# Kernel tuning notes

Hardware: AMD Instinct MI355X
Metric: run time of the kernel (lower is better)

Reference implementation:

```python
import jax, jax.numpy as jnp
import numpy as np


def setup_inputs() -> dict:
    key = jax.random.key(0)
    inputs = jax.random.normal(key, (4, 1024, 64), dtype=jnp.float32)
    return {"inputs": inputs}


def reference(inputs):
    # inputs: (B, N, D)
    # scores[b,i,j] = sum_d tanh(x[b,i,d] + x[b,j,d])
    addition = inputs[:, :, None, :] + inputs[:, None, :, :]  # (B, N, N, D)
    e_values = jnp.tanh(addition).sum(axis=-1)                # (B, N, N)
    weights = jax.nn.softmax(e_values, axis=-1)               # (B, N, N)
    out = jnp.einsum("bij,bjd->bid", weights, inputs)         # (B, N, D)
    return out
```

## Files before the change

### kernel.cpp

```cpp
#include <hip/hip_runtime.h>


#define NB 4
#define NN 1024
#define ND 64
#define TJ 64
#define TI 4
#define NTILES (NN / TJ)

#if __has_builtin(__builtin_amdgcn_exp2f)
#define EXP2F(x) __builtin_amdgcn_exp2f(x)
#else
#define EXP2F(x) exp2f(x)
#endif
#if __has_builtin(__builtin_amdgcn_rcpf)
#define RCPF(x) __builtin_amdgcn_rcpf(x)
#else
#define RCPF(x) (1.0f / (x))
#endif

static constexpr float C_SCALE = 2.8853900817779268f;
static constexpr float K_SHIFT = 46.166241308446828f;

typedef float v2f __attribute__((ext_vector_type(2)));

#define PKFMA(a, b, c) __builtin_elementwise_fma((a), (b), (c))

__device__ __forceinline__ v2f vlo(float4 v) { v2f r; r.x = v.x; r.y = v.y; return r; }
__device__ __forceinline__ v2f vhi(float4 v) { v2f r; r.x = v.z; r.y = v.w; return r; }

__global__ __launch_bounds__(256) void prep_kernel(const float* __restrict__ x,
                                                   float* __restrict__ E) {
    int idx = blockIdx.x * 256 + threadIdx.x;
    float4 v = ((const float4*)x)[idx];
    float4 e;
    e.x = EXP2F(C_SCALE * v.x);
    e.y = EXP2F(C_SCALE * v.y);
    e.z = EXP2F(C_SCALE * v.z);
    e.w = EXP2F(C_SCALE * v.w);
    ((float4*)E)[idx] = e;
}

template <bool HAS_E>
__global__ __launch_bounds__(256, 4) void addattn_kernel(const float* __restrict__ x,
                                                         const float* __restrict__ E,
                                                         float* __restrict__ out) {
    __shared__ float E_lds[TJ * ND];
    __shared__ float x_lds[TJ * ND];

    const int tid   = threadIdx.x;
    const int lane  = tid & 63;
    const int wave  = tid >> 6;
    const int wg    = blockIdx.x;
    const int b     = wg >> 8;
    const int ibase = (wg & 255) * TI;
    const int i0    = __builtin_amdgcn_readfirstlane(ibase + wave);

    const float* xb  = x + (size_t)b * NN * ND;
    const float* Eip = E + (size_t)b * NN * ND + (size_t)i0 * ND;

    float4 px[4];
    {
        const float4* srcx = (const float4*)xb;
        #pragma unroll
        for (int it = 0; it < 4; ++it) px[it] = srcx[it * 256 + tid];
    }

    v2f ei2[32];
    if (!HAS_E) {
        #pragma unroll
        for (int c = 0; c < 16; ++c) {
            float4 xiq = *(const float4*)&xb[(size_t)i0 * ND + c * 4];
            v2f lo, hi;
            lo.x = EXP2F(C_SCALE * xiq.x);
            lo.y = EXP2F(C_SCALE * xiq.y);
            hi.x = EXP2F(C_SCALE * xiq.z);
            hi.y = EXP2F(C_SCALE * xiq.w);
            ei2[2 * c] = lo;
            ei2[2 * c + 1] = hi;
        }
    }

    #pragma unroll
    for (int it = 0; it < 4; ++it) {
        int idx = it * 256 + tid;
        int j   = idx >> 4;
        int c   = idx & 15;
        int wof = j * ND + ((c ^ (j & 15)) << 2);
        *(float4*)&x_lds[wof] = px[it];
        float4 ev;
        ev.x = EXP2F(C_SCALE * px[it].x);
        ev.y = EXP2F(C_SCALE * px[it].y);
        ev.z = EXP2F(C_SCALE * px[it].z);
        ev.w = EXP2F(C_SCALE * px[it].w);
        *(float4*)&E_lds[wof] = ev;
    }
    __syncthreads();

    v2f acc2[32];
    #pragma unroll
    for (int k = 0; k < 32; ++k) acc2[k] = (v2f){0.f, 0.f};
    float dn = 0.f;

    for (int t = 0; t < NTILES; ++t) {
        if (t + 1 < NTILES) {
            const float4* srcx = (const float4*)(xb + (size_t)(t + 1) * TJ * ND);
            #pragma unroll
            for (int it = 0; it < 4; ++it) px[it] = srcx[it * 256 + tid];
        }

        const int key = lane & 15;
        v2f rse = {0.f, 0.f}, rso = {0.f, 0.f};
        #pragma unroll
        for (int c = 0; c < 16; ++c) {
            float4 ejq = *(const float4*)&E_lds[lane * ND + ((c ^ key) << 2)];
            v2f eil, eih;
            if (HAS_E) {
                float4 eiq = *(const float4*)&Eip[c * 4];
                eil = vlo(eiq); eih = vhi(eiq);
            } else {
                eil = ei2[2 * c]; eih = ei2[2 * c + 1];
            }
            v2f a = eil * vlo(ejq);
            v2f q = eih * vhi(ejq);
            v2f p = a + q;
            v2f r = PKFMA(a, q, p + 1.0f);
            v2f tt; tt.x = RCPF(r.x); tt.y = RCPF(r.y);
            if (c & 1) rso = PKFMA(p + 2.0f, tt, rso);
            else       rse = PKFMA(p + 2.0f, tt, rse);
        }
        v2f rs = rse + rso;
        float w = EXP2F(fmaf(-C_SCALE, rs.x + rs.y, K_SHIFT));
        dn += w;
        v2f w2; w2.x = w; w2.y = w;

        #pragma unroll
        for (int c = 0; c < 16; ++c) {
            float4 xq = *(const float4*)&x_lds[lane * ND + ((c ^ key) << 2)];
            acc2[2 * c]     = PKFMA(w2, vlo(xq), acc2[2 * c]);
            acc2[2 * c + 1] = PKFMA(w2, vhi(xq), acc2[2 * c + 1]);
        }

        if (t + 1 < NTILES) {
            __syncthreads();
            #pragma unroll
            for (int it = 0; it < 4; ++it) {
                int idx = it * 256 + tid;
                int j   = idx >> 4;
                int c   = idx & 15;
                int wof = j * ND + ((c ^ (j & 15)) << 2);
                *(float4*)&x_lds[wof] = px[it];
                float4 ev;
                ev.x = EXP2F(C_SCALE * px[it].x);
                ev.y = EXP2F(C_SCALE * px[it].y);
                ev.z = EXP2F(C_SCALE * px[it].z);
                ev.w = EXP2F(C_SCALE * px[it].w);
                *(float4*)&E_lds[wof] = ev;
            }
            __syncthreads();
        }
    }

    float* accf = (float*)acc2;
    #pragma unroll
    for (int s = 0; s < 6; ++s) {
        const int half = 32 >> s;
        const int sel  = (lane >> (5 - s)) & 1;
        #pragma unroll
        for (int k = 0; k < half; ++k) {
            float keep = sel ? accf[k + half] : accf[k];
            float send = sel ? accf[k] : accf[k + half];
            float recv = __shfl_xor(send, half, 64);
            accf[k] = keep + recv;
        }
    }
    #pragma unroll
    for (int s = 0; s < 6; ++s) dn += __shfl_xor(dn, 1 << s, 64);

    out[((size_t)b * NN + i0) * ND + lane] = accf[0] * RCPF(dn);
}

extern "C" void kernel_launch(void* const* d_in, const int* in_sizes, int n_in,
                              void* d_out, int out_size, void* d_ws, size_t ws_size,
                              hipStream_t stream) {
    const float* x = (const float*)d_in[0];
    float* out = (float*)d_out;
    const size_t e_bytes = (size_t)NB * NN * ND * sizeof(float);

    dim3 grid(NB * (NN / TI));
    dim3 block(256);

    if (ws_size >= e_bytes) {
        float* E = (float*)d_ws;
        prep_kernel<<<dim3(NB * NN * ND / 4 / 256), dim3(256), 0, stream>>>(x, E);
        addattn_kernel<true><<<grid, block, 0, stream>>>(x, E, out);
    } else {
        addattn_kernel<false><<<grid, block, 0, stream>>>(x, (const float*)nullptr, out);
    }
}
```

Baseline: 67.98 us.

## Compute exp of sum directly per pair, drop E precompute and LDS tile

```diff
diff --git a/kernel.cpp b/kernel.cpp
--- a/kernel.cpp
+++ b/kernel.cpp
@@ -29,23 +29,8 @@
 __device__ __forceinline__ v2f vlo(float4 v) { v2f r; r.x = v.x; r.y = v.y; return r; }
 __device__ __forceinline__ v2f vhi(float4 v) { v2f r; r.x = v.z; r.y = v.w; return r; }
 
-__global__ __launch_bounds__(256) void prep_kernel(const float* __restrict__ x,
-                                                   float* __restrict__ E) {
-    int idx = blockIdx.x * 256 + threadIdx.x;
-    float4 v = ((const float4*)x)[idx];
-    float4 e;
-    e.x = EXP2F(C_SCALE * v.x);
-    e.y = EXP2F(C_SCALE * v.y);
-    e.z = EXP2F(C_SCALE * v.z);
-    e.w = EXP2F(C_SCALE * v.w);
-    ((float4*)E)[idx] = e;
-}
-
-template <bool HAS_E>
-__global__ __launch_bounds__(256, 4) void addattn_kernel(const float* __restrict__ x,
-                                                         const float* __restrict__ E,
+__global__ __launch_bounds__(256, 2) void addattn_kernel(const float* __restrict__ x,
                                                          float* __restrict__ out) {
-    __shared__ float E_lds[TJ * ND];
     __shared__ float x_lds[TJ * ND];
 
     const int tid   = threadIdx.x;
@@ -57,7 +42,7 @@
     const int i0    = __builtin_amdgcn_readfirstlane(ibase + wave);
 
     const float* xb  = x + (size_t)b * NN * ND;
-    const float* Eip = E + (size_t)b * NN * ND + (size_t)i0 * ND;
+    const float* xip = xb + (size_t)i0 * ND;
 
     float4 px[4];
     {
@@ -65,35 +50,12 @@
         #pragma unroll
         for (int it = 0; it < 4; ++it) px[it] = srcx[it * 256 + tid];
     }
-
-    v2f ei2[32];
-    if (!HAS_E) {
-        #pragma unroll
-        for (int c = 0; c < 16; ++c) {
-            float4 xiq = *(const float4*)&xb[(size_t)i0 * ND + c * 4];
-            v2f lo, hi;
-            lo.x = EXP2F(C_SCALE * xiq.x);
-            lo.y = EXP2F(C_SCALE * xiq.y);
-            hi.x = EXP2F(C_SCALE * xiq.z);
-            hi.y = EXP2F(C_SCALE * xiq.w);
-            ei2[2 * c] = lo;
-            ei2[2 * c + 1] = hi;
-        }
-    }
-
     #pragma unroll
     for (int it = 0; it < 4; ++it) {
         int idx = it * 256 + tid;
         int j   = idx >> 4;
         int c   = idx & 15;
-        int wof = j * ND + ((c ^ (j & 15)) << 2);
-        *(float4*)&x_lds[wof] = px[it];
-        float4 ev;
-        ev.x = EXP2F(C_SCALE * px[it].x);
-        ev.y = EXP2F(C_SCALE * px[it].y);
-        ev.z = EXP2F(C_SCALE * px[it].z);
-        ev.w = EXP2F(C_SCALE * px[it].w);
-        *(float4*)&E_lds[wof] = ev;
+        *(float4*)&x_lds[j * ND + ((c ^ (j & 15)) << 2)] = px[it];
     }
     __syncthreads();
 
@@ -101,6 +63,8 @@
     #pragma unroll
     for (int k = 0; k < 32; ++k) acc2[k] = (v2f){0.f, 0.f};
     float dn = 0.f;
+
+    const v2f C2 = {C_SCALE, C_SCALE};
 
     for (int t = 0; t < NTILES; ++t) {
         if (t + 1 < NTILES) {
@@ -110,21 +74,21 @@
         }
 
         const int key = lane & 15;
+        float4 xjs[16];
         v2f rse = {0.f, 0.f}, rso = {0.f, 0.f};
         #pragma unroll
         for (int c = 0; c < 16; ++c) {
-            float4 ejq = *(const float4*)&E_lds[lane * ND + ((c ^ key) << 2)];
-            v2f eil, eih;
-            if (HAS_E) {
-                float4 eiq = *(const float4*)&Eip[c * 4];
-                eil = vlo(eiq); eih = vhi(eiq);
-            } else {
-                eil = ei2[2 * c]; eih = ei2[2 * c + 1];
-            }
-            v2f a = eil * vlo(ejq);
-            v2f q = eih * vhi(ejq);
-            v2f p = a + q;
-            v2f r = PKFMA(a, q, p + 1.0f);
+            float4 xq = *(const float4*)&x_lds[lane * ND + ((c ^ key) << 2)];
+            asm volatile("" : "+v"(xq.x), "+v"(xq.y), "+v"(xq.z), "+v"(xq.w));
+            xjs[c] = xq;
+            float4 xiq = *(const float4*)&xip[c * 4];
+            v2f Ul = C2 * (vlo(xq) + vlo(xiq));
+            v2f Uh = C2 * (vhi(xq) + vhi(xiq));
+            v2f A, Q;
+            A.x = EXP2F(Ul.x); A.y = EXP2F(Ul.y);
+            Q.x = EXP2F(Uh.x); Q.y = EXP2F(Uh.y);
+            v2f p = A + Q;
+            v2f r = PKFMA(A, Q, p + 1.0f);
             v2f tt; tt.x = RCPF(r.x); tt.y = RCPF(r.y);
             if (c & 1) rso = PKFMA(p + 2.0f, tt, rso);
             else       rse = PKFMA(p + 2.0f, tt, rse);
@@ -136,9 +100,8 @@
 
         #pragma unroll
         for (int c = 0; c < 16; ++c) {
-            float4 xq = *(const float4*)&x_lds[lane * ND + ((c ^ key) << 2)];
-            acc2[2 * c]     = PKFMA(w2, vlo(xq), acc2[2 * c]);
-            acc2[2 * c + 1] = PKFMA(w2, vhi(xq), acc2[2 * c + 1]);
+            acc2[2 * c]     = PKFMA(w2, vlo(xjs[c]), acc2[2 * c]);
+            acc2[2 * c + 1] = PKFMA(w2, vhi(xjs[c]), acc2[2 * c + 1]);
         }
 
         if (t + 1 < NTILES) {
@@ -148,14 +111,7 @@
                 int idx = it * 256 + tid;
                 int j   = idx >> 4;
                 int c   = idx & 15;
-                int wof = j * ND + ((c ^ (j & 15)) << 2);
-                *(float4*)&x_lds[wof] = px[it];
-                float4 ev;
-                ev.x = EXP2F(C_SCALE * px[it].x);
-                ev.y = EXP2F(C_SCALE * px[it].y);
-                ev.z = EXP2F(C_SCALE * px[it].z);
-                ev.w = EXP2F(C_SCALE * px[it].w);
-                *(float4*)&E_lds[wof] = ev;
+                *(float4*)&x_lds[j * ND + ((c ^ (j & 15)) << 2)] = px[it];
             }
             __syncthreads();
         }
@@ -185,16 +141,7 @@
                               hipStream_t stream) {
     const float* x = (const float*)d_in[0];
     float* out = (float*)d_out;
-    const size_t e_bytes = (size_t)NB * NN * ND * sizeof(float);
-
     dim3 grid(NB * (NN / TI));
     dim3 block(256);
-
-    if (ws_size >= e_bytes) {
-        float* E = (float*)d_ws;
-        prep_kernel<<<dim3(NB * NN * ND / 4 / 256), dim3(256), 0, stream>>>(x, E);
-        addattn_kernel<true><<<grid, block, 0, stream>>>(x, E, out);
-    } else {
-        addattn_kernel<false><<<grid, block, 0, stream>>>(x, (const float*)nullptr, out);
-    }
+    addattn_kernel<<<grid, block, 0, stream>>>(x, out);
 }
```

New measurement: 92.42 us. +36.0%, slower.
